# Kernel optimization log

Measured on AMD Instinct MI355X. Metric: run time of the kernel, lower is better.

The kernel has to match this reference:

```python
import jax, jax.numpy as jnp
import numpy as np
from math import sqrt

NUM_HEADS = 16
NUM_KV_HEADS = 4
ROPE_BASE = 10000.0


def setup_inputs() -> dict:
    key = jax.random.key(0)
    ks = jax.random.split(key, 9)
    B, S, E = 4, 2048, 2048
    KV_DIM = NUM_KV_HEADS * (E // NUM_HEADS)  # 512
    s = 0.02
    return {
        "x": jax.random.normal(ks[0], (B, S, E), jnp.float32),
        "wq": jax.random.normal(ks[1], (E, E), jnp.float32) * s,
        "bq": jnp.zeros((E,), jnp.float32),
        "wk": jax.random.normal(ks[2], (KV_DIM, E), jnp.float32) * s,
        "bk": jnp.zeros((KV_DIM,), jnp.float32),
        "wv": jax.random.normal(ks[3], (KV_DIM, E), jnp.float32) * s,
        "bv": jnp.zeros((KV_DIM,), jnp.float32),
        "wo": jax.random.normal(ks[4], (E, E), jnp.float32) * s,
        "bo": jnp.zeros((E,), jnp.float32),
    }


def _rope_cos_sin(seq_len, head_dim, dtype):
    inv_freq = 1.0 / (ROPE_BASE ** (jnp.arange(0, head_dim, 2, dtype=jnp.float32) / head_dim))
    pos = jnp.arange(seq_len, dtype=jnp.float32)
    freqs = pos[:, None] * inv_freq[None, :]            # [S, D/2]
    emb = jnp.concatenate([freqs, freqs], axis=-1)      # [S, D]
    return jnp.cos(emb).astype(dtype), jnp.sin(emb).astype(dtype)


def _apply_rope(t, cos, sin):
    # t: [B, H, S, D]; cos/sin: [S, D]
    d2 = t.shape[-1] // 2
    rot = jnp.concatenate([-t[..., d2:], t[..., :d2]], axis=-1)
    return t * cos[None, None, :, :] + rot * sin[None, None, :, :]


def reference(x, wq, bq, wk, bk, wv, bv, wo, bo):
    B, S, E = x.shape
    H, KV = NUM_HEADS, NUM_KV_HEADS
    D = E // H
    G = H // KV

    q = (x @ wq.T + bq).reshape(B, S, H, D).transpose(0, 2, 1, 3)   # [B,H,S,D]
    k = (x @ wk.T + bk).reshape(B, S, KV, D).transpose(0, 2, 1, 3)  # [B,KV,S,D]
    v = (x @ wv.T + bv).reshape(B, S, KV, D).transpose(0, 2, 1, 3)

    cos, sin = _rope_cos_sin(S, D, x.dtype)
    q = _apply_rope(q, cos, sin)
    k = _apply_rope(k, cos, sin)

    # GQA: expand each kv head group_size times (contiguous repeat)
    k = jnp.repeat(k, G, axis=1)  # [B,H,S,D]
    v = jnp.repeat(v, G, axis=1)

    scores = jnp.einsum("bhqd,bhkd->bhqk", q, k)
    causal = jnp.triu(jnp.ones((S, S), dtype=bool), k=1)
    scores = jnp.where(causal[None, None, :, :], -jnp.inf, scores)
    attn = jax.nn.softmax(scores / sqrt(D), axis=-1)
    out = jnp.einsum("bhqk,bhkd->bhqd", attn, v)        # [B,H,S,D]
    out = out.transpose(0, 2, 1, 3).reshape(B, S, E)
    return out @ wo.T + bo
```

## Files before the change

### kernel.cpp

```cpp
#include <hip/hip_runtime.h>
#include <stdint.h>
#include <math.h>

typedef __attribute__((ext_vector_type(8))) short s16x8;
typedef __attribute__((ext_vector_type(4))) short s16x4;
typedef __attribute__((ext_vector_type(4))) float f32x4;

#define NEGH (-1.0e30f)

__device__ __forceinline__ short f2bf(float f) {
  union { float f; unsigned int i; } c; c.f = f;
  unsigned int lsb = (c.i >> 16) & 1u;
  c.i += 0x7fffu + lsb;
  return (short)(c.i >> 16);
}
__device__ __forceinline__ float bf2f(short u) {
  union { unsigned int i; float f; } c;
  c.i = ((unsigned int)(unsigned short)u) << 16;
  return c.f;
}

#define GLOAD_LDS16(gp, lp)                                                  \
  __builtin_amdgcn_global_load_lds(                                          \
      (__attribute__((address_space(1))) void*)(void*)(gp),                  \
      (__attribute__((address_space(3))) void*)(lp), 16, 0, 0)

__global__ __launch_bounds__(256) void cvt_kernel(const float* __restrict__ in,
                                                  short* __restrict__ out)
{
  const size_t i = ((size_t)blockIdx.x * 256 + threadIdx.x) * 4;
  const float4 v = *(const float4*)(in + i);
  s16x4 o = { f2bf(v.x), f2bf(v.y), f2bf(v.z), f2bf(v.w) };
  *(s16x4*)(out + i) = o;
}

__global__ __launch_bounds__(256) void wcvt_kernel(
    const float* __restrict__ wq, const float* __restrict__ wk,
    const float* __restrict__ wv, short* __restrict__ wqb,
    short* __restrict__ wkb, short* __restrict__ wvb,
    float2* __restrict__ tab)
{
  const int bid = blockIdx.x;
  if (bid < 6144) {
    const float* in; short* out; int lb;
    if (bid < 4096)      { in = wq; out = wqb; lb = bid; }
    else if (bid < 5120) { in = wk; out = wkb; lb = bid - 4096; }
    else                 { in = wv; out = wvb; lb = bid - 5120; }
    const size_t i = ((size_t)lb * 256 + threadIdx.x) * 4;
    const float4 v = *(const float4*)(in + i);
    s16x4 o = { f2bf(v.x), f2bf(v.y), f2bf(v.z), f2bf(v.w) };
    *(s16x4*)(out + i) = o;
  } else {
    const int i = (bid - 6144) * 256 + threadIdx.x;
    const int d = i & 63;
    const float fr = (float)(i >> 6) * exp2f((float)d * -0.20762050593048584f);
    float sn, cs;
    sincosf(fr, &sn, &cs);
    tab[i] = make_float2(cs, sn);
  }
}

__global__ __launch_bounds__(256) void gemm_bt(
    const short* __restrict__ A, const short* __restrict__ W,
    const float* __restrict__ bias, const float* __restrict__ bias2,
    void* __restrict__ C, void* __restrict__ C2,
    int M, int N, int K, int omode)
{
  __shared__ __align__(16) short As[128 * 64];
  __shared__ __align__(16) short Bs[128 * 64];

  const int t = threadIdx.x;
  const int l = t & 63;
  const int w = t >> 6;
  const int lane16 = l & 15;
  const int quad = l >> 4;
  const int wm = w >> 1, wn = w & 1;

  int bx = blockIdx.x, by = blockIdx.y;
  if (gridDim.x == 8 && gridDim.y == 64) {
    const int lid = blockIdx.x + 8 * blockIdx.y;
    const int xcd = lid & 7, idx = lid >> 3;
    by = xcd * 8 + (idx >> 3);
    bx = idx & 7;
  }
  const int mb0 = by * 128;
  const int nb0 = bx * 128;

  const f32x4 zero = {0.f, 0.f, 0.f, 0.f};
  f32x4 acc[4][4];
#pragma unroll
  for (int i = 0; i < 4; ++i)
#pragma unroll
    for (int j = 0; j < 4; ++j) acc[i][j] = zero;

  const int sr = t >> 3;
  const int sp = t & 7;
  const short* Ag = A + (size_t)(mb0 + sr) * K + sp * 8;
  const short* Wg = W + (size_t)(nb0 + sr) * K + sp * 8;
  short* Al = As + t * 8;
  short* Bl = Bs + t * 8;

  const int nkt = K >> 6;
  for (int kt = 0; kt < nkt; ++kt) {
    __syncthreads();
    const int kof = kt * 64;
#pragma unroll
    for (int it = 0; it < 4; ++it) {
      GLOAD_LDS16(Ag + kof + (size_t)(it * 32) * K, Al + it * 2048);
      GLOAD_LDS16(Wg + kof + (size_t)(it * 32) * K, Bl + it * 2048);
    }
    __syncthreads();
#pragma unroll
    for (int kk = 0; kk < 2; ++kk) {
      s16x8 af[4], bf[4];
#pragma unroll
      for (int mi = 0; mi < 4; ++mi)
        af[mi] = *(const s16x8*)&As[(wm * 64 + mi * 16 + lane16) * 64 +
                                    kk * 32 + quad * 8];
#pragma unroll
      for (int ni = 0; ni < 4; ++ni)
        bf[ni] = *(const s16x8*)&Bs[(wn * 64 + ni * 16 + lane16) * 64 +
                                    kk * 32 + quad * 8];
#pragma unroll
      for (int mi = 0; mi < 4; ++mi)
#pragma unroll
        for (int ni = 0; ni < 4; ++ni)
          acc[mi][ni] = __builtin_amdgcn_mfma_f32_16x16x32_bf16(
              af[mi], bf[ni], acc[mi][ni], 0, 0, 0);
    }
  }

#pragma unroll
  for (int ni = 0; ni < 4; ++ni) {
    const int n = nb0 + wn * 64 + ni * 16 + lane16;
    const float bvx = (omode == 3 && n >= 512) ? bias2[n - 512] : bias[n];
#pragma unroll
    for (int mi = 0; mi < 4; ++mi) {
      const int m0 = mb0 + wm * 64 + mi * 16 + quad * 4;
#pragma unroll
      for (int r = 0; r < 4; ++r) {
        const int m = m0 + r;
        const float v = acc[mi][ni][r] + bvx;
        if (omode == 0) {
          ((short*)C)[(size_t)m * N + n] = f2bf(v);
        } else if (omode == 1) {
          ((float*)C)[(size_t)m * N + n] = v;
        } else {
          if (n < 512) ((short*)C)[(size_t)m * 512 + n] = f2bf(v);
          else         ((short*)C2)[(size_t)m * 512 + (n - 512)] = f2bf(v);
        }
      }
    }
  }
}

__global__ __launch_bounds__(512, 2) void gemm256_bt(
    const short* __restrict__ A, const short* __restrict__ W,
    const float* __restrict__ bias, void* __restrict__ C,
    int M, int N, int K, int omode)
{
  __shared__ __align__(16) short Asm[2 * 16384];
  __shared__ __align__(16) short Bsm[2 * 16384];

  const int t = threadIdx.x;
  const int l = t & 63;
  const int w = t >> 6;
  const int lane16 = l & 15;
  const int quad = l >> 4;
  const int wm = w >> 2;
  const int wn = w & 3;

  int bx = blockIdx.x, by = blockIdx.y;
  if (gridDim.x == 8 && gridDim.y == 32) {
    const int bid = blockIdx.y * 8 + blockIdx.x;
    const int xcd = bid & 7, idx = bid >> 3;
    const int xc = xcd & 3, yc = xcd >> 2;
    bx = xc * 2 + (idx & 1);
    by = yc * 16 + (idx >> 1);
  }
  const int mb0 = by * 256;
  const int nb0 = bx * 256;

  const f32x4 zero = {0.f, 0.f, 0.f, 0.f};
  f32x4 acc[8][4];
#pragma unroll
  for (int i = 0; i < 8; ++i)
#pragma unroll
    for (int j = 0; j < 4; ++j) acc[i][j] = zero;

  const int srow = t >> 2;
  const int scs = (t & 3) ^ ((t >> 3) & 3);
  const short* Ag = A + (size_t)(mb0 + srow) * K + scs * 8;
  const short* Wg = W + (size_t)(nb0 + srow) * K + scs * 8;
  const size_t rstep = (size_t)128 * K;

#define STAGE_A(b, kt, kh)                                                    \
  do {                                                                        \
    const size_t ko_ = (size_t)(kt) * 64 + (kh) * 32;                         \
    GLOAD_LDS16(Ag + ko_,         Asm + (b) * 16384 + (kh) * 8192 + t * 8);   \
    GLOAD_LDS16(Ag + ko_ + rstep, Asm + (b) * 16384 + (kh) * 8192 + 4096 + t * 8); \
  } while (0)
#define STAGE_B(b, kt, kh)                                                    \
  do {                                                                        \
    const size_t ko_ = (size_t)(kt) * 64 + (kh) * 32;                         \
    GLOAD_LDS16(Wg + ko_,         Bsm + (b) * 16384 + (kh) * 8192 + t * 8);   \
    GLOAD_LDS16(Wg + ko_ + rstep, Bsm + (b) * 16384 + (kh) * 8192 + 4096 + t * 8); \
  } while (0)

#define VMW6                                                                  \
  asm volatile("s_waitcnt vmcnt(6)" ::: "memory");                            \
  __builtin_amdgcn_sched_barrier(0);

  s16x8 bfr[4];

#define DO_PHASE(BUF, KK, MG, READB, STAGE_STMT, VM_STMT)                     \
  {                                                                           \
    const short* Abase = Asm + (BUF) * 16384 + (KK) * 8192;                   \
    const short* Bbase = Bsm + (BUF) * 16384 + (KK) * 8192;                   \
    if (READB) {                                                              \
      _Pragma("unroll")                                                       \
      for (int ni = 0; ni < 4; ++ni) {                                        \
        const int nr = wn * 64 + ni * 16 + lane16;                            \
        bfr[ni] = *(const s16x8*)(Bbase + nr * 32 +                           \
                                  ((quad ^ ((nr >> 1) & 3)) << 3));           \
      }                                                                       \
    }                                                                         \
    s16x8 afr[4];                                                             \
    _Pragma("unroll")                                                         \
    for (int mi2 = 0; mi2 < 4; ++mi2) {                                       \
      const int mr = wm * 128 + (MG) * 64 + mi2 * 16 + lane16;                \
      afr[mi2] = *(const s16x8*)(Abase + mr * 32 +                            \
                                 ((quad ^ ((mr >> 1) & 3)) << 3));            \
    }                                                                         \
    STAGE_STMT;                                                               \
    __builtin_amdgcn_s_barrier();                                             \
    asm volatile("s_waitcnt lgkmcnt(0)" ::: "memory");                        \
    __builtin_amdgcn_sched_barrier(0);                                        \
    __builtin_amdgcn_s_setprio(1);                                            \
    _Pragma("unroll")                                                         \
    for (int mi2 = 0; mi2 < 4; ++mi2)                                         \
      _Pragma("unroll")                                                       \
      for (int ni = 0; ni < 4; ++ni)                                          \
        acc[(MG) * 4 + mi2][ni] = __builtin_amdgcn_mfma_f32_16x16x32_bf16(    \
            afr[mi2], bfr[ni], acc[(MG) * 4 + mi2][ni], 0, 0, 0);             \
    __builtin_amdgcn_s_setprio(0);                                            \
    VM_STMT                                                                   \
    __builtin_amdgcn_s_barrier();                                             \
  }

  const int NT = K >> 6;

  STAGE_B(0, 0, 0); STAGE_A(0, 0, 0); STAGE_B(0, 0, 1); STAGE_A(0, 0, 1);
  STAGE_B(1, 1, 0); STAGE_A(1, 1, 0); STAGE_B(1, 1, 1);
  asm volatile("s_waitcnt vmcnt(6)" ::: "memory");
  __builtin_amdgcn_sched_barrier(0);
  __builtin_amdgcn_s_barrier();

  for (int i2 = 0; i2 < NT; i2 += 2) {
    const int tp1 = (i2 + 1 < NT) ? i2 + 1 : NT - 1;
    const int tp2 = (i2 + 2 < NT) ? i2 + 2 : NT - 1;
    const int tp3 = (i2 + 3 < NT) ? i2 + 3 : NT - 1;
    DO_PHASE(0, 0, 0, true,  STAGE_A(1, tp1, 1), )
    DO_PHASE(0, 0, 1, false, STAGE_B(0, tp2, 0), )
    DO_PHASE(0, 1, 0, true,  STAGE_A(0, tp2, 0), )
    DO_PHASE(0, 1, 1, false, STAGE_B(0, tp2, 1), VMW6)
    DO_PHASE(1, 0, 0, true,  STAGE_A(0, tp2, 1), )
    DO_PHASE(1, 0, 1, false, STAGE_B(1, tp3, 0), )
    DO_PHASE(1, 1, 0, true,  STAGE_A(1, tp3, 0), )
    DO_PHASE(1, 1, 1, false, STAGE_B(1, tp3, 1), VMW6)
  }

#pragma unroll
  for (int ni = 0; ni < 4; ++ni) {
    const int n = nb0 + wn * 64 + ni * 16 + lane16;
    const float bv = bias[n];
#pragma unroll
    for (int mi = 0; mi < 8; ++mi) {
      const int m0 = mb0 + wm * 128 + mi * 16 + quad * 4;
#pragma unroll
      for (int r = 0; r < 4; ++r) {
        const float v = acc[mi][ni][r] + bv;
        if (omode == 0) ((short*)C)[(size_t)(m0 + r) * N + n] = f2bf(v);
        else            ((float*)C)[(size_t)(m0 + r) * N + n] = v;
      }
    }
  }
#undef DO_PHASE
#undef STAGE_A
#undef STAGE_B
#undef VMW6
}

__global__ __launch_bounds__(256) void rope_kernel(short* __restrict__ buf,
                                                   int lognh,
                                                   const float2* __restrict__ tab)
{
  const int idx = blockIdx.x * 256 + threadIdx.x;
  const int d = idx & 63;
  const int rest = idx >> 6;
  const int row = rest >> lognh;
  const int pos = row & 2047;
  const float2 cssn = tab[(pos << 6) | d];
  const float cs = cssn.x, sn = cssn.y;
  const size_t base = (size_t)rest * 128 + d;
  const float lo = bf2f(buf[base]);
  const float hi = bf2f(buf[base + 64]);
  buf[base]      = f2bf(lo * cs - hi * sn);
  buf[base + 64] = f2bf(hi * cs + lo * sn);
}

__global__ __launch_bounds__(256) void trans_kernel(const short* __restrict__ in,
                                                    short* __restrict__ out)
{
  __shared__ short T[64 * 72];
  const int t = threadIdx.x;
  const int ms = blockIdx.x * 64;
  const int ns = blockIdx.y * 64;
  const int b = ms >> 11;
  const int sl = ms & 2047;
  const int r = t >> 3, sg = t & 7;
#pragma unroll
  for (int j = 0; j < 2; ++j) {
    const uint4 v = *(const uint4*)(in + (size_t)(ms + r + 32 * j) * 512 + ns + sg * 8);
    *(uint4*)&T[(r + 32 * j) * 72 + sg * 8] = v;
  }
  __syncthreads();
#pragma unroll
  for (int j = 0; j < 2; ++j) {
    const int nr = r + 32 * j;
    s16x8 v;
#pragma unroll
    for (int i = 0; i < 8; ++i) v[i] = T[(sg * 8 + i) * 72 + nr];
    *(s16x8*)(out + ((size_t)(b * 512 + ns + nr)) * 2048 + sl + sg * 8) = v;
  }
}

__global__ __launch_bounds__(256, 2) void attn_kernel(
    const short* __restrict__ qg, const short* __restrict__ kg,
    const short* __restrict__ vtg, short* __restrict__ og,
    const float2* __restrict__ tab)
{
  __shared__ __align__(16) short Ksm[2 * 64 * 128];
  __shared__ __align__(16) short Vsm[2 * 128 * 64];
  __shared__ __align__(16) short Psm[128 * 64];

  const int t = threadIdx.x;
  const int l = t & 63;
  const int w = t >> 6;
  const int lane16 = l & 15;
  const int quad = l >> 4;

  const int lid = blockIdx.x + 8 * (blockIdx.y + 16 * blockIdx.z);
  const int xcd = lid & 7, idx = lid >> 3;
  const int g = xcd * 2 + (idx >> 5);
  const int wv_ = idx & 31;
  const int b = g >> 2, kv = g & 3;
  const int h = kv * 4 + (wv_ >> 3);
  const int jb = wv_ & 7;

  const int krow0 = t >> 4, kseg = (t & 15) ^ (krow0 & 7);
  const int vrow0 = t >> 3, vseg = (t & 7) ^ (vrow0 & 7);

  const short* kbaseptr = kg + ((size_t)(b * 2048)) * 512 + kv * 128;
  const short* vbaseptr = vtg + ((size_t)(b * 512 + kv * 128)) * 2048;

  const float SC = 0.08838834764831845f * 1.4426950408889634f;
  const f32x4 zero = {0.f, 0.f, 0.f, 0.f};
  const int swz = (lane16 & 7) << 3;

#define STAGET(c)                                                             \
  do {                                                                        \
    GLOAD_LDS16(ksrc,          Ksm + (c) * 8192 + t * 8);                     \
    GLOAD_LDS16(ksrc + 8192,   Ksm + (c) * 8192 + 2048 + t * 8);              \
    GLOAD_LDS16(ksrc + 16384,  Ksm + (c) * 8192 + 4096 + t * 8);              \
    GLOAD_LDS16(ksrc + 24576,  Ksm + (c) * 8192 + 6144 + t * 8);              \
    GLOAD_LDS16(vsrc,          Vsm + (c) * 8192 + t * 8);                     \
    GLOAD_LDS16(vsrc + 65536,  Vsm + (c) * 8192 + 2048 + t * 8);              \
    GLOAD_LDS16(vsrc + 131072, Vsm + (c) * 8192 + 4096 + t * 8);              \
    GLOAD_LDS16(vsrc + 196608, Vsm + (c) * 8192 + 6144 + t * 8);              \
    ksrc += 64 * 512;                                                         \
    vsrc += 64;                                                               \
  } while (0)

  for (int sp2 = 0; sp2 < 2; ++sp2) {
    const int jj = sp2 ? (15 - jb) : jb;
    const int qb0 = jj * 128;
    const int qw0 = qb0 + w * 32;
    const int qmaxw = qw0 + 31;
    const int ntl = 2 * jj + 2;

    const short* ksrc = kbaseptr + (size_t)krow0 * 512 + kseg * 8;
    const short* vsrc = vbaseptr + (size_t)vrow0 * 2048 + vseg * 8;

    s16x8 qf[2][4];
#pragma unroll
    for (int s = 0; s < 2; ++s) {
      const short* qrow =
          qg + ((size_t)(b * 2048 + qw0 + s * 16 + lane16)) * 2048 + h * 128 + quad * 8;
      s16x8 qr[4];
#pragma unroll
      for (int kk = 0; kk < 4; ++kk) qr[kk] = *(const s16x8*)(qrow + kk * 32);
      const float2* tb = tab + (((size_t)(qw0 + s * 16 + lane16)) << 6) + quad * 8;
#pragma unroll
      for (int kk = 0; kk < 2; ++kk) {
        float lo[8], hi[8];
#pragma unroll
        for (int j = 0; j < 8; ++j) {
          const float2 cs2 = tb[kk * 32 + j];
          const float l0 = bf2f(qr[kk][j]);
          const float h0 = bf2f(qr[kk + 2][j]);
          lo[j] = l0 * cs2.x - h0 * cs2.y;
          hi[j] = h0 * cs2.x + l0 * cs2.y;
        }
        union { unsigned int u[4]; s16x8 v; } plo, phi;
#pragma unroll
        for (int j = 0; j < 4; ++j) {
          asm("v_cvt_pk_bf16_f32 %0, %1, %2"
              : "=v"(plo.u[j]) : "v"(lo[2 * j]), "v"(lo[2 * j + 1]));
          asm("v_cvt_pk_bf16_f32 %0, %1, %2"
              : "=v"(phi.u[j]) : "v"(hi[2 * j]), "v"(hi[2 * j + 1]));
        }
        qf[s][kk] = plo.v;
        qf[s][kk + 2] = phi.v;
      }
    }

    f32x4 o[2][8];
#pragma unroll
    for (int s = 0; s < 2; ++s)
#pragma unroll
      for (int i = 0; i < 8; ++i) o[s][i] = zero;
    float m_i[2] = {NEGH, NEGH};
    float l_i[2] = {0.f, 0.f};

    STAGET(0);
    __syncthreads();
    int cur = 0;

    for (int tl = 0; tl < ntl; ++tl) {
      const int kbase = tl * 64;
      if (tl + 1 < ntl) STAGET(cur ^ 1);

      if (kbase <= qmaxw) {
        const short* Kb = Ksm + cur * 8192;
        const short* Vb = Vsm + cur * 8192;
        f32x4 st[2][4];
#pragma unroll
        for (int s = 0; s < 2; ++s)
#pragma unroll
          for (int mt = 0; mt < 4; ++mt) st[s][mt] = zero;
        __builtin_amdgcn_s_setprio(1);
#pragma unroll
        for (int mt = 0; mt < 4; ++mt) {
          const int rb = (mt * 16 + lane16) * 128;
#pragma unroll
          for (int kk = 0; kk < 4; ++kk) {
            const s16x8 a = *(const s16x8*)&Kb[rb + ((kk * 32 + quad * 8) ^ swz)];
            st[0][mt] = __builtin_amdgcn_mfma_f32_16x16x32_bf16(a, qf[0][kk], st[0][mt], 0, 0, 0);
            st[1][mt] = __builtin_amdgcn_mfma_f32_16x16x32_bf16(a, qf[1][kk], st[1][mt], 0, 0, 0);
          }
        }
        __builtin_amdgcn_s_setprio(0);

        const bool maskt = (kbase + 63 > qw0);
#pragma unroll
        for (int s = 0; s < 2; ++s) {
          const int qabs = qw0 + s * 16 + lane16;
          if (maskt) {
#pragma unroll
            for (int mt = 0; mt < 4; ++mt)
#pragma unroll
              for (int r = 0; r < 4; ++r) {
                if ((kbase + mt * 16 + quad * 4 + r) > qabs) st[s][mt][r] = NEGH;
              }
          }
          float tm[4];
#pragma unroll
          for (int mt = 0; mt < 4; ++mt)
            tm[mt] = fmaxf(fmaxf(st[s][mt][0], st[s][mt][1]),
                           fmaxf(st[s][mt][2], st[s][mt][3]));
          float tl_ = fmaxf(fmaxf(tm[0], tm[1]), fmaxf(tm[2], tm[3]));
          tl_ = fmaxf(tl_, __shfl_xor(tl_, 16));
          tl_ = fmaxf(tl_, __shfl_xor(tl_, 32));
          const float mnew = fmaxf(m_i[s], tl_);
          if (!__all(tl_ <= m_i[s])) {
            const float alpha = exp2f((m_i[s] - mnew) * SC);
            l_i[s] *= alpha;
#pragma unroll
            for (int r = 0; r < 4; ++r) {
              const float ar = __shfl(alpha, quad * 4 + r);
#pragma unroll
              for (int ntd = 0; ntd < 8; ++ntd) o[s][ntd][r] *= ar;
            }
          }
          m_i[s] = mnew;
          const float mS = mnew * SC;
          float rs = 0.f;
#pragma unroll
          for (int mt = 0; mt < 4; ++mt) {
            const float p0 = exp2f(fmaf(st[s][mt][0], SC, -mS));
            const float p1 = exp2f(fmaf(st[s][mt][1], SC, -mS));
            const float p2 = exp2f(fmaf(st[s][mt][2], SC, -mS));
            const float p3 = exp2f(fmaf(st[s][mt][3], SC, -mS));
            rs += (p0 + p1) + (p2 + p3);
            uint2 pk2;
            asm("v_cvt_pk_bf16_f32 %0, %1, %2" : "=v"(pk2.x) : "v"(p0), "v"(p1));
            asm("v_cvt_pk_bf16_f32 %0, %1, %2" : "=v"(pk2.y) : "v"(p2), "v"(p3));
            *(uint2*)&Psm[(w * 32 + s * 16 + lane16) * 64 +
                          ((mt * 16 + quad * 4) ^ swz)] = pk2;
          }
          rs += __shfl_xor(rs, 16);
          rs += __shfl_xor(rs, 32);
          l_i[s] += rs;
        }

        const int prb0 = (w * 32 + lane16) * 64;
        const int prb1 = (w * 32 + 16 + lane16) * 64;
        __builtin_amdgcn_s_setprio(1);
#pragma unroll
        for (int kk = 0; kk < 2; ++kk) {
          const s16x8 pf0 = *(const s16x8*)&Psm[prb0 + ((kk * 32 + quad * 8) ^ swz)];
          const s16x8 pf1 = *(const s16x8*)&Psm[prb1 + ((kk * 32 + quad * 8) ^ swz)];
#pragma unroll
          for (int ntd = 0; ntd < 8; ++ntd) {
            const s16x8 vf =
                *(const s16x8*)&Vb[(ntd * 16 + lane16) * 64 + ((kk * 32 + quad * 8) ^ swz)];
            o[0][ntd] = __builtin_amdgcn_mfma_f32_16x16x32_bf16(pf0, vf, o[0][ntd], 0, 0, 0);
            o[1][ntd] = __builtin_amdgcn_mfma_f32_16x16x32_bf16(pf1, vf, o[1][ntd], 0, 0, 0);
          }
        }
        __builtin_amdgcn_s_setprio(0);
      }

      __syncthreads();
      cur ^= 1;
    }

#pragma unroll
    for (int s = 0; s < 2; ++s)
#pragma unroll
      for (int r = 0; r < 4; ++r) {
        const float lr = __shfl(l_i[s], quad * 4 + r);
        const float inv = 1.f / lr;
        const size_t base =
            ((size_t)(b * 2048 + qw0 + s * 16 + quad * 4 + r)) * 2048 +
            h * 128 + lane16;
#pragma unroll
        for (int ntd = 0; ntd < 8; ++ntd)
          og[base + ntd * 16] = f2bf(o[s][ntd][r] * inv);
      }
  }
#undef STAGET
}

extern "C" void kernel_launch(void* const* d_in, const int* in_sizes, int n_in,
                              void* d_out, int out_size, void* d_ws,
                              size_t ws_size, hipStream_t stream)
{
  const float* x  = (const float*)d_in[0];
  const float* wq = (const float*)d_in[1];
  const float* bq = (const float*)d_in[2];
  const float* wk = (const float*)d_in[3];
  const float* bk = (const float*)d_in[4];
  const float* wv = (const float*)d_in[5];
  const float* bv = (const float*)d_in[6];
  const float* wo = (const float*)d_in[7];
  const float* bo = (const float*)d_in[8];
  float* out = (float*)d_out;

  char* ws = (char*)d_ws;
  short* xb  = (short*)ws;
  short* wqb = (short*)(ws + (32ull << 20));
  short* wkb = (short*)(ws + (40ull << 20));
  short* wvb = (short*)(ws + (42ull << 20));
  short* qws = (short*)(ws + (44ull << 20));
  float2* tab = (float2*)(ws + (76ull << 20));
  short* wob = xb;
  short* kws = (short*)d_out;
  short* vtw = (short*)((char*)d_out + (8ull << 20));
  short* vtmp = (short*)((char*)d_out + (16ull << 20));

  const dim3 blk(256);
  cvt_kernel<<<16384, blk, 0, stream>>>(x, xb);
  wcvt_kernel<<<6656, blk, 0, stream>>>(wq, wk, wv, wqb, wkb, wvb, tab);
  gemm256_bt<<<dim3(8, 32), dim3(512), 0, stream>>>(xb, wqb, bq, qws, 8192, 2048, 2048, 0);
  gemm_bt<<<dim3(8, 64), blk, 0, stream>>>(xb, wkb, bk, bv, kws, vtmp, 8192, 1024, 2048, 3);
  trans_kernel<<<dim3(128, 8), blk, 0, stream>>>(vtmp, vtw);
  rope_kernel<<<8192, blk, 0, stream>>>(kws, 2, tab);
  cvt_kernel<<<4096, blk, 0, stream>>>(wo, wob);
  attn_kernel<<<dim3(8, 16, 4), blk, 0, stream>>>(qws, kws, vtw, qws, tab);
  gemm256_bt<<<dim3(8, 32), dim3(512), 0, stream>>>(qws, wob, bo, out, 8192, 2048, 2048, 1);
}
```

Before: 518.3 us.

## Switch attention to 32x32x16 MFMA and pass P via lane shuffles instead of LDS

The attention kernel now uses 32x32x16 bf16 MFMA tiles for both QK^T and PV. Each wave covers 32 query rows in a single tile rather than two 16-row subtiles. The P matrix is rebuilt in registers with cross-half lane shuffles, so the Psm shared-memory round trip is gone. The K swizzle changes to a 16-way XOR to match the new read pattern. In exchange, the 16-wide accumulators raise register pressure and the code adds shuffle overhead.

```diff
diff --git a/kernel.cpp b/kernel.cpp
--- a/kernel.cpp
+++ b/kernel.cpp
@@ -5,6 +5,7 @@
 typedef __attribute__((ext_vector_type(8))) short s16x8;
 typedef __attribute__((ext_vector_type(4))) short s16x4;
 typedef __attribute__((ext_vector_type(4))) float f32x4;
+typedef __attribute__((ext_vector_type(16))) float f32x16;
 
 #define NEGH (-1.0e30f)
 
@@ -342,13 +343,12 @@
 {
   __shared__ __align__(16) short Ksm[2 * 64 * 128];
   __shared__ __align__(16) short Vsm[2 * 128 * 64];
-  __shared__ __align__(16) short Psm[128 * 64];
 
   const int t = threadIdx.x;
   const int l = t & 63;
   const int w = t >> 6;
-  const int lane16 = l & 15;
-  const int quad = l >> 4;
+  const int l31 = l & 31;
+  const int h2 = l >> 5;
 
   const int lid = blockIdx.x + 8 * (blockIdx.y + 16 * blockIdx.z);
   const int xcd = lid & 7, idx = lid >> 3;
@@ -358,15 +358,15 @@
   const int h = kv * 4 + (wv_ >> 3);
   const int jb = wv_ & 7;
 
-  const int krow0 = t >> 4, kseg = (t & 15) ^ (krow0 & 7);
-  const int vrow0 = t >> 3, vseg = (t & 7) ^ (vrow0 & 7);
+  const int krow0 = t >> 4, kseg = (t & 15) ^ (t >> 4);
+  const int vrow0 = t >> 3, vseg = (t & 7) ^ ((t >> 3) & 7);
 
   const short* kbaseptr = kg + ((size_t)(b * 2048)) * 512 + kv * 128;
   const short* vbaseptr = vtg + ((size_t)(b * 512 + kv * 128)) * 2048;
 
   const float SC = 0.08838834764831845f * 1.4426950408889634f;
-  const f32x4 zero = {0.f, 0.f, 0.f, 0.f};
-  const int swz = (lane16 & 7) << 3;
+  const f32x16 zero16 = {0.f,0.f,0.f,0.f,0.f,0.f,0.f,0.f,
+                         0.f,0.f,0.f,0.f,0.f,0.f,0.f,0.f};
 
 #define STAGET(c)                                                             \
   do {                                                                        \
@@ -392,23 +392,23 @@
     const short* ksrc = kbaseptr + (size_t)krow0 * 512 + kseg * 8;
     const short* vsrc = vbaseptr + (size_t)vrow0 * 2048 + vseg * 8;
 
-    s16x8 qf[2][4];
-#pragma unroll
-    for (int s = 0; s < 2; ++s) {
+    s16x8 qf[8];
+    {
+      const int pos = qw0 + l31;
       const short* qrow =
-          qg + ((size_t)(b * 2048 + qw0 + s * 16 + lane16)) * 2048 + h * 128 + quad * 8;
-      s16x8 qr[4];
-#pragma unroll
-      for (int kk = 0; kk < 4; ++kk) qr[kk] = *(const s16x8*)(qrow + kk * 32);
-      const float2* tb = tab + (((size_t)(qw0 + s * 16 + lane16)) << 6) + quad * 8;
-#pragma unroll
-      for (int kk = 0; kk < 2; ++kk) {
+          qg + ((size_t)(b * 2048 + pos)) * 2048 + h * 128 + 8 * h2;
+      s16x8 qr[8];
+#pragma unroll
+      for (int m = 0; m < 8; ++m) qr[m] = *(const s16x8*)(qrow + 16 * m);
+      const float2* tb = tab + (((size_t)pos) << 6) + 8 * h2;
+#pragma unroll
+      for (int m = 0; m < 4; ++m) {
         float lo[8], hi[8];
 #pragma unroll
         for (int j = 0; j < 8; ++j) {
-          const float2 cs2 = tb[kk * 32 + j];
-          const float l0 = bf2f(qr[kk][j]);
-          const float h0 = bf2f(qr[kk + 2][j]);
+          const float2 cs2 = tb[16 * m + j];
+          const float l0 = bf2f(qr[m][j]);
+          const float h0 = bf2f(qr[m + 4][j]);
           lo[j] = l0 * cs2.x - h0 * cs2.y;
           hi[j] = h0 * cs2.x + l0 * cs2.y;
         }
@@ -420,18 +420,15 @@
           asm("v_cvt_pk_bf16_f32 %0, %1, %2"
               : "=v"(phi.u[j]) : "v"(hi[2 * j]), "v"(hi[2 * j + 1]));
         }
-        qf[s][kk] = plo.v;
-        qf[s][kk + 2] = phi.v;
+        qf[m] = plo.v;
+        qf[m + 4] = phi.v;
       }
     }
 
-    f32x4 o[2][8];
-#pragma unroll
-    for (int s = 0; s < 2; ++s)
-#pragma unroll
-      for (int i = 0; i < 8; ++i) o[s][i] = zero;
-    float m_i[2] = {NEGH, NEGH};
-    float l_i[2] = {0.f, 0.f};
+    f32x16 o32[4];
+#pragma unroll
+    for (int nb = 0; nb < 4; ++nb) o32[nb] = zero16;
+    float m_i = NEGH, l_i = 0.f;
 
     STAGET(0);
     __syncthreads();
@@ -444,89 +441,90 @@
       if (kbase <= qmaxw) {
         const short* Kb = Ksm + cur * 8192;
         const short* Vb = Vsm + cur * 8192;
-        f32x4 st[2][4];
-#pragma unroll
-        for (int s = 0; s < 2; ++s)
-#pragma unroll
-          for (int mt = 0; mt < 4; ++mt) st[s][mt] = zero;
+
+        f32x16 st0 = zero16, st1 = zero16;
         __builtin_amdgcn_s_setprio(1);
 #pragma unroll
-        for (int mt = 0; mt < 4; ++mt) {
-          const int rb = (mt * 16 + lane16) * 128;
-#pragma unroll
-          for (int kk = 0; kk < 4; ++kk) {
-            const s16x8 a = *(const s16x8*)&Kb[rb + ((kk * 32 + quad * 8) ^ swz)];
-            st[0][mt] = __builtin_amdgcn_mfma_f32_16x16x32_bf16(a, qf[0][kk], st[0][mt], 0, 0, 0);
-            st[1][mt] = __builtin_amdgcn_mfma_f32_16x16x32_bf16(a, qf[1][kk], st[1][mt], 0, 0, 0);
+        for (int m = 0; m < 8; ++m) {
+          const int ch = ((2 * m + h2) ^ (l & 15)) * 8;
+          const s16x8 a0 = *(const s16x8*)&Kb[l31 * 128 + ch];
+          const s16x8 a1 = *(const s16x8*)&Kb[(32 + l31) * 128 + ch];
+          st0 = __builtin_amdgcn_mfma_f32_32x32x16_bf16(a0, qf[m], st0, 0, 0, 0);
+          st1 = __builtin_amdgcn_mfma_f32_32x32x16_bf16(a1, qf[m], st1, 0, 0, 0);
+        }
+        __builtin_amdgcn_s_setprio(0);
+
+        const bool maskt = (kbase + 63 > qw0);
+        const int qabs = qw0 + l31;
+        if (maskt) {
+#pragma unroll
+          for (int r = 0; r < 16; ++r) {
+            const int krow = (r & 3) + 8 * (r >> 2) + 4 * h2;
+            if (kbase + krow > qabs) st0[r] = NEGH;
+            if (kbase + 32 + krow > qabs) st1[r] = NEGH;
           }
         }
-        __builtin_amdgcn_s_setprio(0);
-
-        const bool maskt = (kbase + 63 > qw0);
-#pragma unroll
-        for (int s = 0; s < 2; ++s) {
-          const int qabs = qw0 + s * 16 + lane16;
-          if (maskt) {
-#pragma unroll
-            for (int mt = 0; mt < 4; ++mt)
-#pragma unroll
-              for (int r = 0; r < 4; ++r) {
-                if ((kbase + mt * 16 + quad * 4 + r) > qabs) st[s][mt][r] = NEGH;
-              }
+        float tm = NEGH;
+#pragma unroll
+        for (int r = 0; r < 16; ++r) tm = fmaxf(tm, fmaxf(st0[r], st1[r]));
+        float tl_ = fmaxf(tm, __shfl_xor(tm, 32));
+        const float mnew = fmaxf(m_i, tl_);
+        if (!__all(tl_ <= m_i)) {
+          const float alpha = exp2f((m_i - mnew) * SC);
+          l_i *= alpha;
+#pragma unroll
+          for (int r = 0; r < 16; ++r) {
+            const int qrow = (r & 3) + 8 * (r >> 2) + 4 * h2;
+            const float ar = __shfl(alpha, qrow);
+#pragma unroll
+            for (int nb = 0; nb < 4; ++nb) o32[nb][r] *= ar;
           }
-          float tm[4];
-#pragma unroll
-          for (int mt = 0; mt < 4; ++mt)
-            tm[mt] = fmaxf(fmaxf(st[s][mt][0], st[s][mt][1]),
-                           fmaxf(st[s][mt][2], st[s][mt][3]));
-          float tl_ = fmaxf(fmaxf(tm[0], tm[1]), fmaxf(tm[2], tm[3]));
-          tl_ = fmaxf(tl_, __shfl_xor(tl_, 16));
-          tl_ = fmaxf(tl_, __shfl_xor(tl_, 32));
-          const float mnew = fmaxf(m_i[s], tl_);
-          if (!__all(tl_ <= m_i[s])) {
-            const float alpha = exp2f((m_i[s] - mnew) * SC);
-            l_i[s] *= alpha;
-#pragma unroll
-            for (int r = 0; r < 4; ++r) {
-              const float ar = __shfl(alpha, quad * 4 + r);
-#pragma unroll
-              for (int ntd = 0; ntd < 8; ++ntd) o[s][ntd][r] *= ar;
-            }
-          }
-          m_i[s] = mnew;
-          const float mS = mnew * SC;
-          float rs = 0.f;
-#pragma unroll
-          for (int mt = 0; mt < 4; ++mt) {
-            const float p0 = exp2f(fmaf(st[s][mt][0], SC, -mS));
-            const float p1 = exp2f(fmaf(st[s][mt][1], SC, -mS));
-            const float p2 = exp2f(fmaf(st[s][mt][2], SC, -mS));
-            const float p3 = exp2f(fmaf(st[s][mt][3], SC, -mS));
-            rs += (p0 + p1) + (p2 + p3);
-            uint2 pk2;
-            asm("v_cvt_pk_bf16_f32 %0, %1, %2" : "=v"(pk2.x) : "v"(p0), "v"(p1));
-            asm("v_cvt_pk_bf16_f32 %0, %1, %2" : "=v"(pk2.y) : "v"(p2), "v"(p3));
-            *(uint2*)&Psm[(w * 32 + s * 16 + lane16) * 64 +
-                          ((mt * 16 + quad * 4) ^ swz)] = pk2;
-          }
-          rs += __shfl_xor(rs, 16);
-          rs += __shfl_xor(rs, 32);
-          l_i[s] += rs;
-        }
-
-        const int prb0 = (w * 32 + lane16) * 64;
-        const int prb1 = (w * 32 + 16 + lane16) * 64;
+        }
+        m_i = mnew;
+        const float mS = mnew * SC;
+        float rs = 0.f;
+#pragma unroll
+        for (int r = 0; r < 16; ++r) {
+          st0[r] = exp2f(fmaf(st0[r], SC, -mS));
+          st1[r] = exp2f(fmaf(st1[r], SC, -mS));
+          rs += st0[r] + st1[r];
+        }
+        rs += __shfl_xor(rs, 32);
+        l_i += rs;
+
+        unsigned int wA[8], wB[8];
+#pragma unroll
+        for (int a = 0; a < 4; ++a) {
+          asm("v_cvt_pk_bf16_f32 %0, %1, %2"
+              : "=v"(wA[a]) : "v"(st0[4 * a]), "v"(st0[4 * a + 1]));
+          asm("v_cvt_pk_bf16_f32 %0, %1, %2"
+              : "=v"(wB[a]) : "v"(st0[4 * a + 2]), "v"(st0[4 * a + 3]));
+          asm("v_cvt_pk_bf16_f32 %0, %1, %2"
+              : "=v"(wA[a + 4]) : "v"(st1[4 * a]), "v"(st1[4 * a + 1]));
+          asm("v_cvt_pk_bf16_f32 %0, %1, %2"
+              : "=v"(wB[a + 4]) : "v"(st1[4 * a + 2]), "v"(st1[4 * a + 3]));
+        }
+
         __builtin_amdgcn_s_setprio(1);
 #pragma unroll
-        for (int kk = 0; kk < 2; ++kk) {
-          const s16x8 pf0 = *(const s16x8*)&Psm[prb0 + ((kk * 32 + quad * 8) ^ swz)];
-          const s16x8 pf1 = *(const s16x8*)&Psm[prb1 + ((kk * 32 + quad * 8) ^ swz)];
-#pragma unroll
-          for (int ntd = 0; ntd < 8; ++ntd) {
-            const s16x8 vf =
-                *(const s16x8*)&Vb[(ntd * 16 + lane16) * 64 + ((kk * 32 + quad * 8) ^ swz)];
-            o[0][ntd] = __builtin_amdgcn_mfma_f32_16x16x32_bf16(pf0, vf, o[0][ntd], 0, 0, 0);
-            o[1][ntd] = __builtin_amdgcn_mfma_f32_16x16x32_bf16(pf1, vf, o[1][ntd], 0, 0, 0);
+        for (int kk = 0; kk < 4; ++kk) {
+          const int i0 = 2 * (kk & 1) + 4 * (kk >> 1);
+          const unsigned int sA = h2 ? wA[i0] : wA[i0 + 1];
+          const unsigned int sB = h2 ? wB[i0] : wB[i0 + 1];
+          const unsigned int rA = (unsigned int)__shfl_xor((int)sA, 32);
+          const unsigned int rB = (unsigned int)__shfl_xor((int)sB, 32);
+          union { unsigned int u[4]; s16x8 v; } pfu;
+          pfu.u[0] = h2 ? rA : wA[i0];
+          pfu.u[1] = h2 ? rB : wB[i0];
+          pfu.u[2] = h2 ? wA[i0 + 1] : rA;
+          pfu.u[3] = h2 ? wB[i0 + 1] : rB;
+          const s16x8 pf = pfu.v;
+#pragma unroll
+          for (int nb = 0; nb < 4; ++nb) {
+            const s16x8 vf = *(const s16x8*)&Vb[(nb * 32 + l31) * 64 +
+                                                (((2 * kk + h2) ^ (l & 7)) * 8)];
+            o32[nb] = __builtin_amdgcn_mfma_f32_32x32x16_bf16(pf, vf, o32[nb],
+                                                              0, 0, 0);
           }
         }
         __builtin_amdgcn_s_setprio(0);
@@ -537,18 +535,16 @@
     }
 
 #pragma unroll
-    for (int s = 0; s < 2; ++s)
-#pragma unroll
-      for (int r = 0; r < 4; ++r) {
-        const float lr = __shfl(l_i[s], quad * 4 + r);
-        const float inv = 1.f / lr;
-        const size_t base =
-            ((size_t)(b * 2048 + qw0 + s * 16 + quad * 4 + r)) * 2048 +
-            h * 128 + lane16;
-#pragma unroll
-        for (int ntd = 0; ntd < 8; ++ntd)
-          og[base + ntd * 16] = f2bf(o[s][ntd][r] * inv);
-      }
+    for (int r = 0; r < 16; ++r) {
+      const int qrow = (r & 3) + 8 * (r >> 2) + 4 * h2;
+      const float lr = __shfl(l_i, qrow);
+      const float inv = 1.f / lr;
+      const size_t base =
+          ((size_t)(b * 2048 + qw0 + qrow)) * 2048 + h * 128 + l31;
+#pragma unroll
+      for (int nb = 0; nb < 4; ++nb)
+        og[base + nb * 32] = f2bf(o32[nb][r] * inv);
+    }
   }
 #undef STAGET
 }
```

Result: faster. 495.1 us (-4.5%).
